# Kernel tuning notes

Hardware: AMD Instinct MI355X
Metric: run time of the kernel (lower is better)

The kernel has to match this reference:

```python
import jax, jax.numpy as jnp
import numpy as np

B, L, D = 128, 2048, 256
H = 512   # decoder hidden size
U = 256   # attention units

def setup_inputs() -> dict:
    key = jax.random.key(0)
    ks = jax.random.split(key, 8)
    s = lambda fan_in: 1.0 / np.sqrt(fan_in)
    return {
        "features": jax.random.normal(ks[0], (B, L, D), dtype=jnp.float32),
        "hidden": jax.random.normal(ks[1], (B, H), dtype=jnp.float32),
        "W1": jax.random.normal(ks[2], (D, U), dtype=jnp.float32) * s(D),
        "b1": jnp.zeros((U,), dtype=jnp.float32),
        "W2": jax.random.normal(ks[3], (H, U), dtype=jnp.float32) * s(H),
        "b2": jnp.zeros((U,), dtype=jnp.float32),
        "V": jax.random.normal(ks[4], (U, 1), dtype=jnp.float32) * s(U),
        "bV": jnp.zeros((1,), dtype=jnp.float32),
    }

def reference(features, hidden, W1, b1, W2, b2, V, bV):
    # features: [B, L, D], hidden: [B, H]
    proj_f = jnp.einsum('bld,du->blu', features, W1) + b1          # [B, L, U]
    proj_h = (hidden @ W2 + b2)[:, None, :]                         # [B, 1, U]
    score = jnp.tanh(proj_f + proj_h)                               # [B, L, U]
    logits = jnp.einsum('blu,uo->blo', score, V) + bV               # [B, L, 1]
    attention_weights = jax.nn.softmax(logits, axis=1)              # [B, L, 1]
    context_vector = jnp.sum(attention_weights * features, axis=1)  # [B, D]
    return context_vector, attention_weights
```

## Files before the change

kernel.cpp:

```cpp
#include <hip/hip_runtime.h>
#include <hip/hip_bf16.h>

#define B_ 128
#define L_ 2048
#define D_ 256
#define H_ 512
#define U_ 256

typedef _Float16 half8 __attribute__((ext_vector_type(8)));
typedef float f32x4 __attribute__((ext_vector_type(4)));

__global__ __launch_bounds__(256) void kp_w1split(
    const float* __restrict__ W1, _Float16* __restrict__ W1t_hi,
    _Float16* __restrict__ W1t_lo) {
  int k = blockIdx.x;
  int u = threadIdx.x;
  float x = W1[k * U_ + u];
  _Float16 hi = (_Float16)x;
  _Float16 lo = (_Float16)(x - (float)hi);
  W1t_hi[u * D_ + k] = hi;
  W1t_lo[u * D_ + k] = lo;
}

__global__ __launch_bounds__(256) void ka_proj_h(
    const float* __restrict__ hidden, const float* __restrict__ W2,
    const float* __restrict__ b1, const float* __restrict__ b2,
    float* __restrict__ ph) {
  int b = blockIdx.x;
  int u = threadIdx.x;
  __shared__ float hs[H_];
  for (int k = u; k < H_; k += 256) hs[k] = hidden[b * H_ + k];
  __syncthreads();
  float acc = b1[u] + b2[u];
#pragma unroll 8
  for (int k = 0; k < H_; ++k) acc += hs[k] * W2[k * U_ + u];
  ph[b * U_ + u] = acc;
}

#define TLM 64
#define BKC 32

__global__ __launch_bounds__(256, 2) void kb_mfma(
    const float* __restrict__ features, const _Float16* __restrict__ W1t_hi,
    const _Float16* __restrict__ W1t_lo, const float* __restrict__ ph,
    const float* __restrict__ V, float* __restrict__ logits) {
  __shared__ __align__(16) _Float16 Ah[TLM][40], Al[TLM][40];
  __shared__ __align__(16) _Float16 Bh[U_][40], Bl[U_][40];
  __shared__ float red[4][TLM];

  const int tid = threadIdx.x;
  const int w = tid >> 6;
  const int lane = tid & 63;
  const int g = lane >> 4;
  const int c = lane & 15;
  const int bidx = blockIdx.x;
  const int b = bidx >> 5;
  const int l0 = (bidx & 31) * TLM;
  const int wcol0 = w * 64;
  const float* fbase = features + ((size_t)b * L_ + l0) * D_;

  f32x4 acc[4][4];
#pragma unroll
  for (int mt = 0; mt < 4; ++mt)
#pragma unroll
    for (int nt = 0; nt < 4; ++nt) acc[mt][nt] = (f32x4){0.f, 0.f, 0.f, 0.f};

  for (int kc = 0; kc < D_; kc += BKC) {
#pragma unroll
    for (int j = 0; j < 2; ++j) {
      int idx = tid + j * 256;
      int row = idx >> 3;
      int c4 = idx & 7;
      float4 x = *(const float4*)&fbase[(size_t)row * D_ + kc + c4 * 4];
      union { _Float16 h[4]; float2 f; } hh, ll;
      hh.h[0] = (_Float16)x.x; ll.h[0] = (_Float16)(x.x - (float)hh.h[0]);
      hh.h[1] = (_Float16)x.y; ll.h[1] = (_Float16)(x.y - (float)hh.h[1]);
      hh.h[2] = (_Float16)x.z; ll.h[2] = (_Float16)(x.z - (float)hh.h[2]);
      hh.h[3] = (_Float16)x.w; ll.h[3] = (_Float16)(x.w - (float)hh.h[3]);
      *(float2*)&Ah[row][c4 * 4] = hh.f;
      *(float2*)&Al[row][c4 * 4] = ll.f;
    }
#pragma unroll
    for (int j = 0; j < 4; ++j) {
      int idx = tid + j * 256;
      int row = idx >> 2;
      int q = idx & 3;
      *(float4*)&Bh[row][q * 8] =
          *(const float4*)&W1t_hi[(size_t)row * D_ + kc + q * 8];
      *(float4*)&Bl[row][q * 8] =
          *(const float4*)&W1t_lo[(size_t)row * D_ + kc + q * 8];
    }
    __syncthreads();

    half8 ah[4], al[4];
#pragma unroll
    for (int mt = 0; mt < 4; ++mt) {
      ah[mt] = *(const half8*)&Ah[mt * 16 + c][g * 8];
      al[mt] = *(const half8*)&Al[mt * 16 + c][g * 8];
    }
#pragma unroll
    for (int nt = 0; nt < 4; ++nt) {
      half8 bh = *(const half8*)&Bh[wcol0 + nt * 16 + c][g * 8];
      half8 bl = *(const half8*)&Bl[wcol0 + nt * 16 + c][g * 8];
#pragma unroll
      for (int mt = 0; mt < 4; ++mt) {
        acc[mt][nt] =
            __builtin_amdgcn_mfma_f32_16x16x32_f16(ah[mt], bh, acc[mt][nt], 0, 0, 0);
        acc[mt][nt] =
            __builtin_amdgcn_mfma_f32_16x16x32_f16(ah[mt], bl, acc[mt][nt], 0, 0, 0);
        acc[mt][nt] =
            __builtin_amdgcn_mfma_f32_16x16x32_f16(al[mt], bh, acc[mt][nt], 0, 0, 0);
      }
    }
    __syncthreads();
  }

  float phv[4], vv[4];
#pragma unroll
  for (int nt = 0; nt < 4; ++nt) {
    int col = wcol0 + nt * 16 + c;
    phv[nt] = ph[b * U_ + col];
    vv[nt] = V[col];
  }
#pragma unroll
  for (int mt = 0; mt < 4; ++mt) {
#pragma unroll
    for (int j = 0; j < 4; ++j) {
      float part = 0.f;
#pragma unroll
      for (int nt = 0; nt < 4; ++nt) {
        float x = acc[mt][nt][j] + phv[nt];
        float e = __expf(2.f * x);
        float t = 1.f - 2.f * __builtin_amdgcn_rcpf(e + 1.f);
        part += t * vv[nt];
      }
      part += __shfl_xor(part, 1, 16);
      part += __shfl_xor(part, 2, 16);
      part += __shfl_xor(part, 4, 16);
      part += __shfl_xor(part, 8, 16);
      if (c == 0) red[w][mt * 16 + g * 4 + j] = part;
    }
  }
  __syncthreads();
  if (tid < TLM) {
    logits[b * L_ + l0 + tid] =
        red[0][tid] + red[1][tid] + red[2][tid] + red[3][tid];
  }
}

__global__ __launch_bounds__(256) void kc_softmax(
    const float* __restrict__ logits, float* __restrict__ wout) {
  int b = blockIdx.x;
  int tid = threadIdx.x;
  const float* lrow = logits + b * L_;
  float v[8];
  *(float4*)&v[0] = *(const float4*)&lrow[tid * 8];
  *(float4*)&v[4] = *(const float4*)&lrow[tid * 8 + 4];

  float m = v[0];
#pragma unroll
  for (int i = 1; i < 8; ++i) m = fmaxf(m, v[i]);
#pragma unroll
  for (int off = 1; off <= 32; off <<= 1) m = fmaxf(m, __shfl_xor(m, off, 64));
  __shared__ float sm[4];
  if ((tid & 63) == 0) sm[tid >> 6] = m;
  __syncthreads();
  m = fmaxf(fmaxf(sm[0], sm[1]), fmaxf(sm[2], sm[3]));

  float s = 0.f;
#pragma unroll
  for (int i = 0; i < 8; ++i) {
    v[i] = __expf(v[i] - m);
    s += v[i];
  }
#pragma unroll
  for (int off = 1; off <= 32; off <<= 1) s += __shfl_xor(s, off, 64);
  __shared__ float ss[4];
  if ((tid & 63) == 0) ss[tid >> 6] = s;
  __syncthreads();
  s = ss[0] + ss[1] + ss[2] + ss[3];

  float inv = 1.f / s;
#pragma unroll
  for (int i = 0; i < 8; ++i) v[i] *= inv;
  *(float4*)&wout[b * L_ + tid * 8] = *(float4*)&v[0];
  *(float4*)&wout[b * L_ + tid * 8 + 4] = *(float4*)&v[4];
}

__global__ __launch_bounds__(256) void kd_partial(
    const float* __restrict__ features, const float* __restrict__ w,
    float* __restrict__ partials) {
  int bidx = blockIdx.x;
  int b = bidx >> 3;
  int chunk = bidx & 7;
  int tid = threadIdx.x;
  int lq = tid >> 6;
  int dq = tid & 63;
  __shared__ float wsm[256];
  wsm[tid] = w[b * L_ + chunk * 256 + tid];
  __syncthreads();
  const float* fb =
      features + ((size_t)b * L_ + chunk * 256 + lq * 64) * D_ + dq * 4;
  const float* wl = &wsm[lq * 64];
  float4 acc = {0.f, 0.f, 0.f, 0.f};
#pragma unroll 8
  for (int i = 0; i < 64; ++i) {
    float wt = wl[i];
    float4 fv = *(const float4*)(fb + (size_t)i * D_);
    acc.x += wt * fv.x;
    acc.y += wt * fv.y;
    acc.z += wt * fv.z;
    acc.w += wt * fv.w;
  }
  __shared__ float red[4][256];
  *(float4*)&red[lq][dq * 4] = acc;
  __syncthreads();
  float ssum = red[0][tid] + red[1][tid] + red[2][tid] + red[3][tid];
  partials[(size_t)(b * 8 + chunk) * 256 + tid] = ssum;
}

__global__ __launch_bounds__(256) void ke_reduce(
    const float* __restrict__ partials, float* __restrict__ ctx) {
  int b = blockIdx.x;
  int d = threadIdx.x;
  float s = 0.f;
#pragma unroll
  for (int c = 0; c < 8; ++c) s += partials[(size_t)(b * 8 + c) * 256 + d];
  ctx[b * 256 + d] = s;
}

extern "C" void kernel_launch(void* const* d_in, const int* in_sizes, int n_in,
                              void* d_out, int out_size, void* d_ws,
                              size_t ws_size, hipStream_t stream) {
  const float* features = (const float*)d_in[0];
  const float* hidden = (const float*)d_in[1];
  const float* W1 = (const float*)d_in[2];
  const float* b1 = (const float*)d_in[3];
  const float* W2 = (const float*)d_in[4];
  const float* b2 = (const float*)d_in[5];
  const float* V = (const float*)d_in[6];

  float* ws = (float*)d_ws;
  float* ph = ws;
  float* logits = ws + 32768;
  float* partials = ws + 32768 + 262144;
  _Float16* W1t_hi = (_Float16*)(ws + 557056);
  _Float16* W1t_lo = W1t_hi + 65536;

  float* ctx = (float*)d_out;
  float* wout = (float*)d_out + B_ * D_;

  kp_w1split<<<D_, 256, 0, stream>>>(W1, W1t_hi, W1t_lo);
  ka_proj_h<<<B_, 256, 0, stream>>>(hidden, W2, b1, b2, ph);
  kb_mfma<<<B_ * (L_ / TLM), 256, 0, stream>>>(features, W1t_hi, W1t_lo, ph, V,
                                               logits);
  kc_softmax<<<B_, 256, 0, stream>>>(logits, wout);
  kd_partial<<<B_ * 8, 256, 0, stream>>>(features, wout, partials);
  ke_reduce<<<B_, 256, 0, stream>>>(partials, ctx);
}
```

Measured before the change: 505.6 us.

## Double-buffer W1 tiles via direct global-to-LDS loads and prefetch features

```diff
diff --git a/kernel.cpp b/kernel.cpp
--- a/kernel.cpp
+++ b/kernel.cpp
@@ -10,16 +10,27 @@
 typedef _Float16 half8 __attribute__((ext_vector_type(8)));
 typedef float f32x4 __attribute__((ext_vector_type(4)));
 
+__device__ __forceinline__ void gll16(const void* gsrc, void* lds) {
+  __builtin_amdgcn_global_load_lds(
+      (const __attribute__((address_space(1))) unsigned int*)gsrc,
+      (__attribute__((address_space(3))) unsigned int*)lds, 16, 0, 0);
+}
+
 __global__ __launch_bounds__(256) void kp_w1split(
-    const float* __restrict__ W1, _Float16* __restrict__ W1t_hi,
-    _Float16* __restrict__ W1t_lo) {
-  int k = blockIdx.x;
+    const float* __restrict__ W1, _Float16* __restrict__ hi,
+    _Float16* __restrict__ lo) {
+  int slot = blockIdx.x;
   int u = threadIdx.x;
-  float x = W1[k * U_ + u];
-  _Float16 hi = (_Float16)x;
-  _Float16 lo = (_Float16)(x - (float)hi);
-  W1t_hi[u * D_ + k] = hi;
-  W1t_lo[u * D_ + k] = lo;
+  union { _Float16 h[8]; float4 f; } H, Lo;
+#pragma unroll
+  for (int j = 0; j < 8; ++j) {
+    float x = W1[(slot * 8 + j) * U_ + u];
+    _Float16 h = (_Float16)x;
+    H.h[j] = h;
+    Lo.h[j] = (_Float16)(x - (float)h);
+  }
+  *(float4*)&hi[((size_t)slot * U_ + u) * 8] = H.f;
+  *(float4*)&lo[((size_t)slot * U_ + u) * 8] = Lo.f;
 }
 
 __global__ __launch_bounds__(256) void ka_proj_h(
@@ -39,13 +50,14 @@
 
 #define TLM 64
 #define BKC 32
+#define NCH (D_ / BKC)
 
 __global__ __launch_bounds__(256, 2) void kb_mfma(
-    const float* __restrict__ features, const _Float16* __restrict__ W1t_hi,
-    const _Float16* __restrict__ W1t_lo, const float* __restrict__ ph,
+    const float* __restrict__ features, const _Float16* __restrict__ W1s_hi,
+    const _Float16* __restrict__ W1s_lo, const float* __restrict__ ph,
     const float* __restrict__ V, float* __restrict__ logits) {
-  __shared__ __align__(16) _Float16 Ah[TLM][40], Al[TLM][40];
-  __shared__ __align__(16) _Float16 Bh[U_][40], Bl[U_][40];
+  __shared__ __align__(16) _Float16 Ah[4][TLM][8], Al[4][TLM][8];
+  __shared__ __align__(16) _Float16 Bh[2][4][U_][8], Bl[2][4][U_][8];
   __shared__ float red[4][TLM];
 
   const int tid = threadIdx.x;
@@ -53,66 +65,101 @@
   const int lane = tid & 63;
   const int g = lane >> 4;
   const int c = lane & 15;
-  const int bidx = blockIdx.x;
-  const int b = bidx >> 5;
-  const int l0 = (bidx & 31) * TLM;
+  const int b = blockIdx.x >> 5;
+  const int l0 = (blockIdx.x & 31) * TLM;
   const int wcol0 = w * 64;
   const float* fbase = features + ((size_t)b * L_ + l0) * D_;
 
+  const int ar = tid & 63;
+  const int ag = tid >> 6;
+  const float* aptr = fbase + ar * D_ + ag * 8;
+
+  _Float16* bhb[2] = {&Bh[0][0][0][0], &Bh[1][0][0][0]};
+  _Float16* blb[2] = {&Bl[0][0][0][0], &Bl[1][0][0][0]};
+#define STAGE_B(t, buf)                                                     \
+  do {                                                                      \
+    const size_t roff = (size_t)(t) * 4 * U_ * 8;          \
+    _Pragma("unroll") for (int q = 0; q < 4; ++q) {                         \
+      const int poff = (w * 4 + q) * 512;                       \
+      gll16(W1s_hi + roff + poff + lane * 8, bhb[buf] + poff);              \
+      gll16(W1s_lo + roff + poff + lane * 8, blb[buf] + poff);              \
+    }                                                                       \
+  } while (0)
+
+#define CONV_WRITE_A(a0, a1)                                                \
+  do {                                                                      \
+    union { _Float16 h[8]; float4 f; } H, Lo;                               \
+    H.h[0] = (_Float16)a0.x; Lo.h[0] = (_Float16)(a0.x - (float)H.h[0]);    \
+    H.h[1] = (_Float16)a0.y; Lo.h[1] = (_Float16)(a0.y - (float)H.h[1]);    \
+    H.h[2] = (_Float16)a0.z; Lo.h[2] = (_Float16)(a0.z - (float)H.h[2]);    \
+    H.h[3] = (_Float16)a0.w; Lo.h[3] = (_Float16)(a0.w - (float)H.h[3]);    \
+    H.h[4] = (_Float16)a1.x; Lo.h[4] = (_Float16)(a1.x - (float)H.h[4]);    \
+    H.h[5] = (_Float16)a1.y; Lo.h[5] = (_Float16)(a1.y - (float)H.h[5]);    \
+    H.h[6] = (_Float16)a1.z; Lo.h[6] = (_Float16)(a1.z - (float)H.h[6]);    \
+    H.h[7] = (_Float16)a1.w; Lo.h[7] = (_Float16)(a1.w - (float)H.h[7]);    \
+    *(float4*)&Ah[ag][ar][0] = H.f;                                         \
+    *(float4*)&Al[ag][ar][0] = Lo.f;                                        \
+  } while (0)
+
   f32x4 acc[4][4];
 #pragma unroll
   for (int mt = 0; mt < 4; ++mt)
 #pragma unroll
     for (int nt = 0; nt < 4; ++nt) acc[mt][nt] = (f32x4){0.f, 0.f, 0.f, 0.f};
 
-  for (int kc = 0; kc < D_; kc += BKC) {
-#pragma unroll
-    for (int j = 0; j < 2; ++j) {
-      int idx = tid + j * 256;
-      int row = idx >> 3;
-      int c4 = idx & 7;
-      float4 x = *(const float4*)&fbase[(size_t)row * D_ + kc + c4 * 4];
-      union { _Float16 h[4]; float2 f; } hh, ll;
-      hh.h[0] = (_Float16)x.x; ll.h[0] = (_Float16)(x.x - (float)hh.h[0]);
-      hh.h[1] = (_Float16)x.y; ll.h[1] = (_Float16)(x.y - (float)hh.h[1]);
-      hh.h[2] = (_Float16)x.z; ll.h[2] = (_Float16)(x.z - (float)hh.h[2]);
-      hh.h[3] = (_Float16)x.w; ll.h[3] = (_Float16)(x.w - (float)hh.h[3]);
-      *(float2*)&Ah[row][c4 * 4] = hh.f;
-      *(float2*)&Al[row][c4 * 4] = ll.f;
-    }
-#pragma unroll
-    for (int j = 0; j < 4; ++j) {
-      int idx = tid + j * 256;
-      int row = idx >> 2;
-      int q = idx & 3;
-      *(float4*)&Bh[row][q * 8] =
-          *(const float4*)&W1t_hi[(size_t)row * D_ + kc + q * 8];
-      *(float4*)&Bl[row][q * 8] =
-          *(const float4*)&W1t_lo[(size_t)row * D_ + kc + q * 8];
-    }
+  {
+    STAGE_B(0, 0);
+    float4 a0 = *(const float4*)(aptr);
+    float4 a1 = *(const float4*)(aptr + 4);
+    CONV_WRITE_A(a0, a1);
+  }
+  __syncthreads();
+
+#pragma unroll
+  for (int t = 0; t < NCH; ++t) {
+    const int buf = t & 1;
+    float4 a0, a1;
+    if (t < NCH - 1) {
+      a0 = *(const float4*)(aptr + (t + 1) * BKC);
+      a1 = *(const float4*)(aptr + (t + 1) * BKC + 4);
+      STAGE_B(t + 1, buf ^ 1);
+    }
+
+    half8 ah[4], al[4], bh[4], bl[4];
+#pragma unroll
+    for (int mt = 0; mt < 4; ++mt) {
+      ah[mt] = *(const half8*)&Ah[g][mt * 16 + c][0];
+      al[mt] = *(const half8*)&Al[g][mt * 16 + c][0];
+    }
+#pragma unroll
+    for (int nt = 0; nt < 4; ++nt) {
+      bh[nt] = *(const half8*)&Bh[buf][g][wcol0 + nt * 16 + c][0];
+      bl[nt] = *(const half8*)&Bl[buf][g][wcol0 + nt * 16 + c][0];
+    }
+#pragma unroll
+    for (int nt = 0; nt < 4; ++nt)
+#pragma unroll
+      for (int mt = 0; mt < 4; ++mt)
+        acc[mt][nt] = __builtin_amdgcn_mfma_f32_16x16x32_f16(ah[mt], bh[nt],
+                                                             acc[mt][nt], 0, 0, 0);
+#pragma unroll
+    for (int nt = 0; nt < 4; ++nt)
+#pragma unroll
+      for (int mt = 0; mt < 4; ++mt)
+        acc[mt][nt] = __builtin_amdgcn_mfma_f32_16x16x32_f16(ah[mt], bl[nt],
+                                                             acc[mt][nt], 0, 0, 0);
+#pragma unroll
+    for (int nt = 0; nt < 4; ++nt)
+#pragma unroll
+      for (int mt = 0; mt < 4; ++mt)
+        acc[mt][nt] = __builtin_amdgcn_mfma_f32_16x16x32_f16(al[mt], bh[nt],
+                                                             acc[mt][nt], 0, 0, 0);
+
     __syncthreads();
-
-    half8 ah[4], al[4];
-#pragma unroll
-    for (int mt = 0; mt < 4; ++mt) {
-      ah[mt] = *(const half8*)&Ah[mt * 16 + c][g * 8];
-      al[mt] = *(const half8*)&Al[mt * 16 + c][g * 8];
-    }
-#pragma unroll
-    for (int nt = 0; nt < 4; ++nt) {
-      half8 bh = *(const half8*)&Bh[wcol0 + nt * 16 + c][g * 8];
-      half8 bl = *(const half8*)&Bl[wcol0 + nt * 16 + c][g * 8];
-#pragma unroll
-      for (int mt = 0; mt < 4; ++mt) {
-        acc[mt][nt] =
-            __builtin_amdgcn_mfma_f32_16x16x32_f16(ah[mt], bh, acc[mt][nt], 0, 0, 0);
-        acc[mt][nt] =
-            __builtin_amdgcn_mfma_f32_16x16x32_f16(ah[mt], bl, acc[mt][nt], 0, 0, 0);
-        acc[mt][nt] =
-            __builtin_amdgcn_mfma_f32_16x16x32_f16(al[mt], bh, acc[mt][nt], 0, 0, 0);
-      }
-    }
-    __syncthreads();
+    if (t < NCH - 1) {
+      CONV_WRITE_A(a0, a1);
+      __syncthreads();
+    }
   }
 
   float phv[4], vv[4];
@@ -131,8 +178,8 @@
       for (int nt = 0; nt < 4; ++nt) {
         float x = acc[mt][nt][j] + phv[nt];
         float e = __expf(2.f * x);
-        float t = 1.f - 2.f * __builtin_amdgcn_rcpf(e + 1.f);
-        part += t * vv[nt];
+        float tnh = 1.f - 2.f * __builtin_amdgcn_rcpf(e + 1.f);
+        part += tnh * vv[nt];
       }
       part += __shfl_xor(part, 1, 16);
       part += __shfl_xor(part, 2, 16);
@@ -146,6 +193,8 @@
     logits[b * L_ + l0 + tid] =
         red[0][tid] + red[1][tid] + red[2][tid] + red[3][tid];
   }
+#undef STAGE_B
+#undef CONV_WRITE_A
 }
 
 __global__ __launch_bounds__(256) void kc_softmax(
@@ -244,15 +293,15 @@
   float* ph = ws;
   float* logits = ws + 32768;
   float* partials = ws + 32768 + 262144;
-  _Float16* W1t_hi = (_Float16*)(ws + 557056);
-  _Float16* W1t_lo = W1t_hi + 65536;
+  _Float16* W1s_hi = (_Float16*)(ws + 557056);
+  _Float16* W1s_lo = W1s_hi + 65536;
 
   float* ctx = (float*)d_out;
   float* wout = (float*)d_out + B_ * D_;
 
-  kp_w1split<<<D_, 256, 0, stream>>>(W1, W1t_hi, W1t_lo);
+  kp_w1split<<<D_ / 8, 256, 0, stream>>>(W1, W1s_hi, W1s_lo);
   ka_proj_h<<<B_, 256, 0, stream>>>(hidden, W2, b1, b2, ph);
-  kb_mfma<<<B_ * (L_ / TLM), 256, 0, stream>>>(features, W1t_hi, W1t_lo, ph, V,
+  kb_mfma<<<B_ * (L_ / TLM), 256, 0, stream>>>(features, W1s_hi, W1s_lo, ph, V,
                                                logits);
   kc_softmax<<<B_, 256, 0, stream>>>(logits, wout);
   kd_partial<<<B_ * 8, 256, 0, stream>>>(features, wout, partials);
```

Result: slower. 540.2 us (+6.8%).
